# Performance work log

Measured on AMD Instinct MI355X. Metric: run time of the kernel, lower is better.

## Reference

```python
import jax, jax.numpy as jnp
import numpy as np

B, T, D = 2, 2048, 1024
NH, NKV, HD = 16, 4, 64
ROPE = 16  # partial RoPE dims (first 16 of 64)
HALF = ROPE // 2


def apply_rope(x, cos, sin):
    # x: (B, nH, T, HD); rotate first ROPE dims, pass the rest through
    x1 = x[..., :HALF]
    x2 = x[..., HALF:ROPE]
    xp = x[..., ROPE:]
    c = cos[None, None, :, :]  # (1,1,T,HALF)
    s = sin[None, None, :, :]
    return jnp.concatenate([x1 * c - x2 * s, x1 * s + x2 * c, xp], axis=-1)


def setup_inputs() -> dict:
    key = jax.random.key(0)
    k0, k1, k2 = jax.random.split(key, 3)
    x = jax.random.normal(k0, (B, T, D), dtype=jnp.float32)
    # RoPE tables for the rotated sub-dimension (half = ROPE//2 = 8)
    inv_freq = 1.0 / (10000.0 ** (jnp.arange(HALF, dtype=jnp.float32) / HALF))
    ang = jnp.arange(T, dtype=jnp.float32)[:, None] * inv_freq[None, :]
    cos = jnp.cos(ang)
    sin = jnp.sin(ang)
    attn_mask = jnp.tril(jnp.ones((T, T), dtype=bool))  # causal
    w_qkv = jax.random.normal(k1, ((NH + 2 * NKV) * HD, D), dtype=jnp.float32) * (D ** -0.5)
    w_out = jax.random.normal(k2, (D, D), dtype=jnp.float32) * (D ** -0.5)
    q_scale = jnp.full((NH, 1), 1.5, dtype=jnp.float32)
    k_scale = jnp.full((NKV, 1), 1.5, dtype=jnp.float32)
    return {"x": x, "cos": cos, "sin": sin, "attn_mask": attn_mask,
            "w_qkv": w_qkv, "w_out": w_out, "q_scale": q_scale, "k_scale": k_scale}


def reference(x, cos, sin, attn_mask, w_qkv, w_out, q_scale, k_scale):
    Bx, Tx, C = x.shape
    groups = NH // NKV
    qkv = x @ w_qkv.T  # (B,T,(NH+2*NKV)*HD)
    q, k, v = jnp.split(qkv, [NH * HD, (NH + NKV) * HD], axis=-1)
    q = q.reshape(Bx, Tx, NH, HD).transpose(0, 2, 1, 3)    # (B,NH,T,HD)
    k = k.reshape(Bx, Tx, NKV, HD).transpose(0, 2, 1, 3)   # (B,NKV,T,HD)
    v = v.reshape(Bx, Tx, NKV, HD).transpose(0, 2, 1, 3)
    # per-head qk gain scaling
    q = q * q_scale[None, :, :, None]  # (1,NH,1,1)
    k = k * k_scale[None, :, :, None]
    # partial RoPE on q and k
    q = apply_rope(q, cos[:Tx], sin[:Tx])
    k = apply_rope(k, cos[:Tx], sin[:Tx])
    # GQA expand (repeat_interleave along heads)
    ke = jnp.repeat(k, groups, axis=1)  # (B,NH,T,HD)
    ve = jnp.repeat(v, groups, axis=1)
    # scaled dot-product attention with causal mask
    scores = jnp.einsum('bhqd,bhkd->bhqk', q, ke) * (HD ** -0.5)
    scores = jnp.where(attn_mask[None, None], scores, -jnp.inf)
    probs = jax.nn.softmax(scores, axis=-1)
    ao = jnp.einsum('bhqk,bhkd->bhqd', probs, ve)  # (B,NH,T,HD)
    # xsa: subtract self-component along the (shared) kv value direction
    ao_r = ao.reshape(Bx, NKV, groups, Tx, HD)
    vv = v[:, :, None]  # (B,NKV,1,T,HD), broadcasts over groups
    dots = jnp.sum(ao_r * vv, axis=-1, keepdims=True)
    norm = jnp.maximum(jnp.sum(vv * vv, axis=-1, keepdims=True), 1e-8)
    ao = (ao_r - (dots / norm) * vv).reshape(Bx, NH, Tx, HD)
    out = ao.transpose(0, 2, 1, 3).reshape(Bx, Tx, C) @ w_out.T
    return out
```

## Files before the change

kernel.cpp:

```cpp
#include <hip/hip_runtime.h>
#include <hip/hip_bf16.h>

#define NB 2
#define NT 2048
#define ND 1024
#define NHEADS 16
#define NKVH 4
#define HDIM 64
#define QKVD 1536

typedef __attribute__((ext_vector_type(8))) short short8;
typedef __attribute__((ext_vector_type(4))) float floatx4;

#if defined(__has_builtin)
#  if __has_builtin(__builtin_amdgcn_global_load_lds)
#    define HAS_GLL 1
#  endif
#endif
#ifndef HAS_GLL
#  define HAS_GLL 0
#endif

__device__ __forceinline__ void gll16(const void* g, void* l, int lane) {
#if HAS_GLL
  (void)lane;
  __builtin_amdgcn_global_load_lds(
      (const __attribute__((address_space(1))) unsigned int*)g,
      (__attribute__((address_space(3))) unsigned int*)l, 16, 0, 0);
#else
  *(short8*)((short*)l) = *(const short8*)g;
#endif
}

__device__ __forceinline__ unsigned short f2bf(float f) {
  union { float f; unsigned int u; } cv; cv.f = f;
  unsigned int u = cv.u;
  u += 0x7fffu + ((u >> 16) & 1u);
  return (unsigned short)(u >> 16);
}
__device__ __forceinline__ float bf2f(unsigned short u) {
  union { unsigned int u; float f; } cv; cv.u = ((unsigned int)u) << 16; return cv.f;
}

#define N4_X   1048576
#define N4_WQ   393216
#define N4_WO   262144
__global__ __launch_bounds__(256) void cvt_all(
    const float* __restrict__ x, const float* __restrict__ wq,
    const float* __restrict__ wo,
    unsigned short* __restrict__ xb, unsigned short* __restrict__ wqb,
    unsigned short* __restrict__ wob) {
  int i = blockIdx.x * 256 + threadIdx.x;
  const float* src; unsigned short* dst; int j;
  if (i < N4_X)              { src = x;  dst = xb;  j = i; }
  else if (i < N4_X + N4_WQ) { src = wq; dst = wqb; j = i - N4_X; }
  else                       { src = wo; dst = wob; j = i - N4_X - N4_WQ; }
  float4 v = ((const float4*)src)[j];
  ushort4 o;
  o.x = f2bf(v.x); o.y = f2bf(v.y); o.z = f2bf(v.z); o.w = f2bf(v.w);
  ((ushort4*)dst)[j] = o;
}

__global__ __launch_bounds__(256) void gemm_qkv(
    const unsigned short* __restrict__ A,
    const unsigned short* __restrict__ Bm,
    const float* __restrict__ cosT, const float* __restrict__ sinT,
    const float* __restrict__ q_scale, const float* __restrict__ k_scale,
    unsigned short* __restrict__ qb, unsigned short* __restrict__ kb,
    unsigned short* __restrict__ vtb)
{
  const int M = NB * NT, N = QKVD, K = ND;
  __shared__ __align__(16) short As[2][128][32];
  __shared__ __align__(16) short Bs[2][128][32];

  const int tid = threadIdx.x;
  const int wid = tid >> 6, lane = tid & 63;
  const int quad = lane >> 4, l16 = lane & 15;
  const int lo8 = l16 & 7;
  const int wm = (wid >> 1) * 64, wn = (wid & 1) * 64;
  const int m0 = blockIdx.x * 128, n0 = blockIdx.y * 128;

  const int r0 = tid >> 2;
  const int lc = ((tid & 3) ^ (r0 & 3)) * 8;

  const unsigned short* ag0 = A  + (size_t)(m0 + r0) * K + lc;
  const unsigned short* ag1 = ag0 + (size_t)64 * K;
  const unsigned short* bg0 = Bm + (size_t)(n0 + r0) * K + lc;
  const unsigned short* bg1 = bg0 + (size_t)64 * K;

  short* asb = &As[0][0][0];
  short* bsb = &Bs[0][0][0];
  const int lofs = (HAS_GLL ? wid * 512 : tid * 8);
  const int cs = (quad ^ (l16 & 3)) * 8;

  floatx4 acc[4][4] = {};

  gll16(ag0, asb + lofs, lane);
  gll16(ag1, asb + 2048 + lofs, lane);
  gll16(bg0, bsb + lofs, lane);
  gll16(bg1, bsb + 2048 + lofs, lane);

  const int NIT = K / 32;
  for (int it = 0; it < NIT; it++) {
    __syncthreads();
    const int bi = it & 1, bn = bi ^ 1;
    if (it + 1 < NIT) {
      const int k = (it + 1) * 32;
      gll16(ag0 + k, asb + bn * 4096 + lofs, lane);
      gll16(ag1 + k, asb + bn * 4096 + 2048 + lofs, lane);
      gll16(bg0 + k, bsb + bn * 4096 + lofs, lane);
      gll16(bg1 + k, bsb + bn * 4096 + 2048 + lofs, lane);
    }
    short8 af[4], bf[4];
#pragma unroll
    for (int mi = 0; mi < 4; mi++) af[mi] = *(const short8*)&As[bi][wm + mi * 16 + l16][cs];
#pragma unroll
    for (int ni = 0; ni < 4; ni++) bf[ni] = *(const short8*)&Bs[bi][wn + ni * 16 + l16][cs];
#pragma unroll
    for (int mi = 0; mi < 4; mi++)
#pragma unroll
      for (int ni = 0; ni < 4; ni++)
        acc[mi][ni] = __builtin_amdgcn_mfma_f32_16x16x32_bf16(af[mi], bf[ni], acc[mi][ni], 0, 0, 0);
  }

  const int hh = blockIdx.y * 2 + (wid & 1);

  if (hh >= NHEADS + NKVH) {
    const int kvh = hh - (NHEADS + NKVH);
#pragma unroll
    for (int mi = 0; mi < 4; mi++) {
      const int mrow = m0 + wm + mi * 16 + quad * 4;
      const int bb = mrow >> 11, tt = mrow & (NT - 1);
#pragma unroll
      for (int ni = 0; ni < 4; ni++) {
        const int d = ni * 16 + l16;
        ushort4 w;
        w.x = f2bf(acc[mi][ni][0]); w.y = f2bf(acc[mi][ni][1]);
        w.z = f2bf(acc[mi][ni][2]); w.w = f2bf(acc[mi][ni][3]);
        *(ushort4*)(vtb + ((size_t)((bb * NKVH + kvh) * HDIM + d)) * NT + tt) = w;
      }
    }
  } else {
    float scl; unsigned short* dst0; int hloc;
    if (hh < NHEADS) { scl = q_scale[hh] * (0.125f * 1.44269504088896f); hloc = hh; dst0 = qb; }
    else             { scl = k_scale[hh - NHEADS];                        hloc = hh - NHEADS; dst0 = kb; }
    const int nh = (hh < NHEADS) ? NHEADS : NKVH;
#pragma unroll
    for (int mi = 0; mi < 4; mi++) {
#pragma unroll
      for (int r = 0; r < 4; r++) {
        const int mrow = m0 + wm + mi * 16 + quad * 4 + r;
        const int bb = mrow >> 11, tt = mrow & (NT - 1);
        unsigned short* drow = dst0 + ((size_t)((bb * nh + hloc) * NT + tt)) * HDIM;

        const float own = acc[mi][0][r];
        const float oth = __shfl_xor(own, 8);
        const float c = cosT[tt * 8 + lo8], s = sinT[tt * 8 + lo8];
        const float roped = (l16 < 8) ? (own * c - oth * s)
                                      : (oth * s + own * c);
        drow[l16] = f2bf(roped * scl);
#pragma unroll
        for (int ni = 1; ni < 4; ni++)
          drow[ni * 16 + l16] = f2bf(acc[mi][ni][r] * scl);
      }
    }
  }
}

__global__ __launch_bounds__(256) void gemm_lds(
    const unsigned short* __restrict__ A,
    const unsigned short* __restrict__ Bm,
    float* __restrict__ C, int M, int N, int K)
{
  __shared__ __align__(16) short As[2][128][32];
  __shared__ __align__(16) short Bs[2][128][32];

  const int tid = threadIdx.x;
  const int wid = tid >> 6, lane = tid & 63;
  const int quad = lane >> 4, l16 = lane & 15;
  const int wm = (wid >> 1) * 64, wn = (wid & 1) * 64;
  const int m0 = blockIdx.x * 128, n0 = blockIdx.y * 128;

  const int r0 = tid >> 2;
  const int lc = ((tid & 3) ^ (r0 & 3)) * 8;

  const unsigned short* ag0 = A  + (size_t)(m0 + r0) * K + lc;
  const unsigned short* ag1 = ag0 + (size_t)64 * K;
  const unsigned short* bg0 = Bm + (size_t)(n0 + r0) * K + lc;
  const unsigned short* bg1 = bg0 + (size_t)64 * K;

  short* asb = &As[0][0][0];
  short* bsb = &Bs[0][0][0];
  const int lofs = (HAS_GLL ? wid * 512 : tid * 8);
  const int cs = (quad ^ (l16 & 3)) * 8;

  floatx4 acc[4][4] = {};

  gll16(ag0, asb + lofs, lane);
  gll16(ag1, asb + 2048 + lofs, lane);
  gll16(bg0, bsb + lofs, lane);
  gll16(bg1, bsb + 2048 + lofs, lane);

  const int NIT = K / 32;
  for (int it = 0; it < NIT; it++) {
    __syncthreads();
    const int bi = it & 1, bn = bi ^ 1;
    if (it + 1 < NIT) {
      const int k = (it + 1) * 32;
      gll16(ag0 + k, asb + bn * 4096 + lofs, lane);
      gll16(ag1 + k, asb + bn * 4096 + 2048 + lofs, lane);
      gll16(bg0 + k, bsb + bn * 4096 + lofs, lane);
      gll16(bg1 + k, bsb + bn * 4096 + 2048 + lofs, lane);
    }
    short8 af[4], bf[4];
#pragma unroll
    for (int mi = 0; mi < 4; mi++) af[mi] = *(const short8*)&As[bi][wm + mi * 16 + l16][cs];
#pragma unroll
    for (int ni = 0; ni < 4; ni++) bf[ni] = *(const short8*)&Bs[bi][wn + ni * 16 + l16][cs];
#pragma unroll
    for (int mi = 0; mi < 4; mi++)
#pragma unroll
      for (int ni = 0; ni < 4; ni++)
        acc[mi][ni] = __builtin_amdgcn_mfma_f32_16x16x32_bf16(af[mi], bf[ni], acc[mi][ni], 0, 0, 0);
  }

#pragma unroll
  for (int mi = 0; mi < 4; mi++)
#pragma unroll
    for (int ni = 0; ni < 4; ni++)
#pragma unroll
      for (int r = 0; r < 4; r++) {
        int m = m0 + wm + mi * 16 + quad * 4 + r;
        int n = n0 + wn + ni * 16 + l16;
        C[(size_t)m * N + n] = acc[mi][ni][r];
      }
}

__global__ __launch_bounds__(256) void fattn(
    const unsigned short* __restrict__ qb,
    const unsigned short* __restrict__ kb,
    const unsigned short* __restrict__ vtb,
    unsigned short* __restrict__ aob,
    float* __restrict__ pbuf)
{
  const int idx = blockIdx.x;
  const int h = blockIdx.y, b = blockIdx.z;
  const int kv = h >> 2;

  int qt, j0, cnt, chunk; bool direct;
  if (idx < 16) { qt = 16 + idx; j0 = 0; cnt = 16; chunk = 0; direct = false; }
  else {
    int rel = idx - 16, s = 16 - (rel >> 1);
    if ((rel & 1) == 0) { qt = s - 1;  j0 = 0;  cnt = s; chunk = 0; direct = true;  }
    else                { qt = s + 15; j0 = 16; cnt = s; chunk = 1; direct = false; }
  }

  const int tid = threadIdx.x;
  const int wid = tid >> 6, lane = tid & 63;
  const int quad = lane >> 4, l16 = lane & 15;
  const int hi8 = l16 >> 3, lo8 = l16 & 7;

  __shared__ __align__(16) short Ks[2][64][64];
  __shared__ __align__(16) short Vs[2][64][64];
  __shared__ __align__(16) short Ps[4][16][64];

  const unsigned short* qg = qb + ((size_t)((b * NHEADS + h) * NT + qt * 64)) * HDIM;
  const int qrow = wid * 16 + l16;
  short8 aq0 = *(const short8*)(qg + (size_t)qrow * HDIM + quad * 8);
  short8 aq1 = *(const short8*)(qg + (size_t)qrow * HDIM + 32 + quad * 8);

  const int sr  = tid >> 3;
  const int lck = ((tid & 7) ^ (sr & 7)) * 8;
  const unsigned short* kgp0 = kb  + ((size_t)((b * NKVH + kv) * NT) + sr) * HDIM + lck;
  const unsigned short* vgp0 = vtb + ((size_t)((b * NKVH + kv) * HDIM) + sr) * NT + lck;
  short* ksb = &Ks[0][0][0];
  short* vsb = &Vs[0][0][0];
  const int lofs = (HAS_GLL ? wid * 512 : tid * 8);

  const int cs0 = (quad ^ lo8) * 8;
  const int cs1 = cs0 ^ 32;

  int pwo[4][4];
#pragma unroll
  for (int r = 0; r < 4; r++) {
    const int row = quad * 4 + r;
#pragma unroll
    for (int nb = 0; nb < 4; nb++)
      pwo[r][nb] = wid * 1024 + row * 64 + (((nb * 2 + hi8) ^ (row & 7)) * 8) + lo8;
  }
  short* psf = &Ps[0][0][0];

  floatx4 acc_o[4] = {};
  float lsum[4] = {0.f, 0.f, 0.f, 0.f};

  {
    const unsigned short* kg = kgp0 + (size_t)j0 * 64 * HDIM;
    const unsigned short* vg = vgp0 + j0 * 64;
    gll16(kg, ksb + lofs, lane);
    gll16(kg + 32 * HDIM, ksb + 2048 + lofs, lane);
    gll16(vg, vsb + lofs, lane);
    gll16(vg + (size_t)32 * NT, vsb + 2048 + lofs, lane);
  }

  for (int i = 0; i < cnt; i++) {
    const int jt = j0 + i;
    __syncthreads();
    const int bi = i & 1, bn = bi ^ 1;
    if (i + 1 < cnt) {
      const unsigned short* kg = kgp0 + (size_t)(jt + 1) * 64 * HDIM;
      const unsigned short* vg = vgp0 + (jt + 1) * 64;
      gll16(kg, ksb + bn * 4096 + lofs, lane);
      gll16(kg + 32 * HDIM, ksb + bn * 4096 + 2048 + lofs, lane);
      gll16(vg, vsb + bn * 4096 + lofs, lane);
      gll16(vg + (size_t)32 * NT, vsb + bn * 4096 + 2048 + lofs, lane);
    }

    floatx4 s[4] = {};
#pragma unroll
    for (int nb = 0; nb < 4; nb++) {
      short8 bk0 = *(const short8*)&Ks[bi][nb * 16 + l16][cs0];
      short8 bk1 = *(const short8*)&Ks[bi][nb * 16 + l16][cs1];
      s[nb] = __builtin_amdgcn_mfma_f32_16x16x32_bf16(aq0, bk0, s[nb], 0, 0, 0);
      s[nb] = __builtin_amdgcn_mfma_f32_16x16x32_bf16(aq1, bk1, s[nb], 0, 0, 0);
    }

    if (jt == qt) {
#pragma unroll
      for (int nb = 0; nb < 4; nb++) {
        int col = nb * 16 + l16;
#pragma unroll
        for (int r = 0; r < 4; r++)
          if (col > wid * 16 + quad * 4 + r) s[nb][r] = -INFINITY;
      }
    }

#pragma unroll
    for (int r = 0; r < 4; r++) {
#pragma unroll
      for (int nb = 0; nb < 4; nb++) {
        float p = __builtin_amdgcn_exp2f(s[nb][r]);
        lsum[r] += p;
        psf[pwo[r][nb]] = (short)(__float_as_uint(p) >> 16);
      }
    }

    short8 ap0 = *(const short8*)&Ps[wid][l16][cs0];
    short8 ap1 = *(const short8*)&Ps[wid][l16][cs1];
#pragma unroll
    for (int nb = 0; nb < 4; nb++) {
      short8 bv0 = *(const short8*)&Vs[bi][nb * 16 + l16][cs0];
      short8 bv1 = *(const short8*)&Vs[bi][nb * 16 + l16][cs1];
      acc_o[nb] = __builtin_amdgcn_mfma_f32_16x16x32_bf16(ap0, bv0, acc_o[nb], 0, 0, 0);
      acc_o[nb] = __builtin_amdgcn_mfma_f32_16x16x32_bf16(ap1, bv1, acc_o[nb], 0, 0, 0);
    }
  }

  const int bl = (cnt - 1) & 1;

  if (direct) {
#pragma unroll
    for (int r = 0; r < 4; r++) {
      float ls = lsum[r];
#pragma unroll
      for (int off = 1; off < 16; off <<= 1) ls += __shfl_xor(ls, off);
      const float invl = 1.f / ls;

      const int rowl = wid * 16 + quad * 4 + r;
      const int vcol = ((rowl >> 3) ^ lo8) * 8 + (rowl & 7);
      float vd[4], dot = 0.f, vv = 0.f;
#pragma unroll
      for (int nb = 0; nb < 4; nb++) {
        vd[nb] = bf2f((unsigned short)Vs[bl][nb * 16 + l16][vcol]);
        dot += acc_o[nb][r] * invl * vd[nb];
        vv  += vd[nb] * vd[nb];
      }
#pragma unroll
      for (int off = 1; off < 16; off <<= 1) {
        dot += __shfl_xor(dot, off);
        vv  += __shfl_xor(vv, off);
      }
      const float coef = dot / fmaxf(vv, 1e-8f);
      unsigned short* dst = aob + ((size_t)(b * NT + qt * 64 + rowl)) * ND + h * HDIM + l16;
#pragma unroll
      for (int nb = 0; nb < 4; nb++)
        dst[nb * 16] = f2bf(acc_o[nb][r] * invl - coef * vd[nb]);
    }
  } else {
    const int slot = ((b * NHEADS + h) * 16 + (qt - 16)) * 2 + chunk;
    float* pO = pbuf + (size_t)slot * 4160;
    float* pl = pO + 4096;
#pragma unroll
    for (int r = 0; r < 4; r++) {
      float ls = lsum[r];
#pragma unroll
      for (int off = 1; off < 16; off <<= 1) ls += __shfl_xor(ls, off);
      const int rowl = wid * 16 + quad * 4 + r;
      if (l16 == 0) pl[rowl] = ls;
#pragma unroll
      for (int nb = 0; nb < 4; nb++)
        pO[rowl * 64 + nb * 16 + l16] = acc_o[nb][r];
    }
  }
}

__global__ __launch_bounds__(256) void redn(
    const float* __restrict__ pbuf,
    const unsigned short* __restrict__ vtb,
    unsigned short* __restrict__ aob)
{
  const int qt = 16 + blockIdx.x;
  const int h = blockIdx.y, b = blockIdx.z;
  const int kv = h >> 2;
  const int tid = threadIdx.x;

  const int slot0 = ((b * NHEADS + h) * 16 + blockIdx.x) * 2;
  const float* O0 = pbuf + (size_t)slot0 * 4160;
  const float* O1 = O0 + 4160;
  const float* l0 = O0 + 4096;
  const float* l1 = O1 + 4096;

  __shared__ short vt[64][66];

  {
    const int d = tid >> 2, tq = (tid & 3) * 16;
    const unsigned short* src = vtb + ((size_t)((b * NKVH + kv) * HDIM + d)) * NT + qt * 64 + tq;
    short8 v0 = *(const short8*)src;
    short8 v1 = *(const short8*)(src + 8);
    *(short8*)&vt[d][tq] = v0;
    *(short8*)&vt[d][tq + 8] = v1;
  }
  __syncthreads();

  const int row = tid >> 2, dq = tid & 3;
  const float invl = 1.f / (l0[row] + l1[row]);

  float o[16], vd[16];
  float dot = 0.f, vv = 0.f;
#pragma unroll
  for (int j = 0; j < 16; j++) {
    const int d = dq * 16 + j;
    float ov = (O0[row * 64 + d] + O1[row * 64 + d]) * invl;
    float v  = bf2f((unsigned short)vt[d][row]);
    o[j] = ov; vd[j] = v;
    dot += ov * v; vv += v * v;
  }
  dot += __shfl_xor(dot, 1); dot += __shfl_xor(dot, 2);
  vv  += __shfl_xor(vv, 1);  vv  += __shfl_xor(vv, 2);
  const float coef = dot / fmaxf(vv, 1e-8f);

  unsigned short* dst = aob + ((size_t)(b * NT + qt * 64 + row)) * ND + h * HDIM + dq * 16;
  ushort4 w0, w1, w2, w3;
  w0.x = f2bf(o[0] - coef * vd[0]);  w0.y = f2bf(o[1] - coef * vd[1]);
  w0.z = f2bf(o[2] - coef * vd[2]);  w0.w = f2bf(o[3] - coef * vd[3]);
  w1.x = f2bf(o[4] - coef * vd[4]);  w1.y = f2bf(o[5] - coef * vd[5]);
  w1.z = f2bf(o[6] - coef * vd[6]);  w1.w = f2bf(o[7] - coef * vd[7]);
  w2.x = f2bf(o[8] - coef * vd[8]);  w2.y = f2bf(o[9] - coef * vd[9]);
  w2.z = f2bf(o[10] - coef * vd[10]); w2.w = f2bf(o[11] - coef * vd[11]);
  w3.x = f2bf(o[12] - coef * vd[12]); w3.y = f2bf(o[13] - coef * vd[13]);
  w3.z = f2bf(o[14] - coef * vd[14]); w3.w = f2bf(o[15] - coef * vd[15]);
  ((ushort4*)dst)[0] = w0; ((ushort4*)dst)[1] = w1;
  ((ushort4*)dst)[2] = w2; ((ushort4*)dst)[3] = w3;
}

extern "C" void kernel_launch(void* const* d_in, const int* in_sizes, int n_in,
                              void* d_out, int out_size, void* d_ws, size_t ws_size,
                              hipStream_t stream) {
  const float* x       = (const float*)d_in[0];
  const float* cosT    = (const float*)d_in[1];
  const float* sinT    = (const float*)d_in[2];
  const float* w_qkv   = (const float*)d_in[4];
  const float* w_out   = (const float*)d_in[5];
  const float* q_scale = (const float*)d_in[6];
  const float* k_scale = (const float*)d_in[7];
  float* out = (float*)d_out;

  char* ws = (char*)d_ws;
  unsigned short* xb    = (unsigned short*)ws;
  unsigned short* wqkvb = (unsigned short*)(ws + 8388608);
  float*          pbuf  = (float*)ws;
  unsigned short* woutb = (unsigned short*)(ws + 17825792);
  unsigned short* qb    = (unsigned short*)(ws + 19922944);
  unsigned short* kb    = (unsigned short*)(ws + 28311552);
  unsigned short* vtb   = (unsigned short*)(ws + 30408704);
  unsigned short* aob   = (unsigned short*)(ws + 32505856);

  cvt_all<<<(N4_X + N4_WQ + N4_WO) / 256, 256, 0, stream>>>(
      x, w_qkv, w_out, xb, wqkvb, woutb);

  gemm_qkv<<<dim3(NB * NT / 128, QKVD / 128), 256, 0, stream>>>(
      xb, wqkvb, cosT, sinT, q_scale, k_scale, qb, kb, vtb);

  fattn<<<dim3(48, NHEADS, NB), 256, 0, stream>>>(qb, kb, vtb, aob, pbuf);
  redn<<<dim3(16, NHEADS, NB), 256, 0, stream>>>(pbuf, vtb, aob);

  gemm_lds<<<dim3(NB * NT / 128, ND / 128), 256, 0, stream>>>(
      aob, woutb, out, NB * NT, ND, ND);
}
```

Measured before the change: 195.2 us.

## Shrink GEMM N-tiles to 64 and pair query heads per attention block

Both GEMMs now use 128x64 tiles in which each wave owns 32 rows across the full 64 columns, which doubles the grid and gives the 256-CU part more blocks. The QKV GEMM now maps one head per block column. The attention kernel now has each block handle two query heads that share a KV head, with each wave doing 32 query rows, so every K/V tile staged in LDS is used by twice as many MFMAs. The trade-off is fewer attention blocks, twice the Ps LDS footprint, and more registers per wave, which may lower occupancy.

```diff
diff --git a/kernel.cpp b/kernel.cpp
--- a/kernel.cpp
+++ b/kernel.cpp
@@ -69,16 +69,16 @@
     unsigned short* __restrict__ qb, unsigned short* __restrict__ kb,
     unsigned short* __restrict__ vtb)
 {
-  const int M = NB * NT, N = QKVD, K = ND;
+  const int K = ND;
   __shared__ __align__(16) short As[2][128][32];
-  __shared__ __align__(16) short Bs[2][128][32];
+  __shared__ __align__(16) short Bs[2][64][32];
 
   const int tid = threadIdx.x;
   const int wid = tid >> 6, lane = tid & 63;
   const int quad = lane >> 4, l16 = lane & 15;
   const int lo8 = l16 & 7;
-  const int wm = (wid >> 1) * 64, wn = (wid & 1) * 64;
-  const int m0 = blockIdx.x * 128, n0 = blockIdx.y * 128;
+  const int wm = wid * 32;
+  const int m0 = blockIdx.x * 128, n0 = blockIdx.y * 64;
 
   const int r0 = tid >> 2;
   const int lc = ((tid & 3) ^ (r0 & 3)) * 8;
@@ -86,19 +86,17 @@
   const unsigned short* ag0 = A  + (size_t)(m0 + r0) * K + lc;
   const unsigned short* ag1 = ag0 + (size_t)64 * K;
   const unsigned short* bg0 = Bm + (size_t)(n0 + r0) * K + lc;
-  const unsigned short* bg1 = bg0 + (size_t)64 * K;
 
   short* asb = &As[0][0][0];
   short* bsb = &Bs[0][0][0];
   const int lofs = (HAS_GLL ? wid * 512 : tid * 8);
   const int cs = (quad ^ (l16 & 3)) * 8;
 
-  floatx4 acc[4][4] = {};
+  floatx4 acc[2][4] = {};
 
   gll16(ag0, asb + lofs, lane);
   gll16(ag1, asb + 2048 + lofs, lane);
   gll16(bg0, bsb + lofs, lane);
-  gll16(bg1, bsb + 2048 + lofs, lane);
 
   const int NIT = K / 32;
   for (int it = 0; it < NIT; it++) {
@@ -108,27 +106,26 @@
       const int k = (it + 1) * 32;
       gll16(ag0 + k, asb + bn * 4096 + lofs, lane);
       gll16(ag1 + k, asb + bn * 4096 + 2048 + lofs, lane);
-      gll16(bg0 + k, bsb + bn * 4096 + lofs, lane);
-      gll16(bg1 + k, bsb + bn * 4096 + 2048 + lofs, lane);
-    }
-    short8 af[4], bf[4];
-#pragma unroll
-    for (int mi = 0; mi < 4; mi++) af[mi] = *(const short8*)&As[bi][wm + mi * 16 + l16][cs];
-#pragma unroll
-    for (int ni = 0; ni < 4; ni++) bf[ni] = *(const short8*)&Bs[bi][wn + ni * 16 + l16][cs];
-#pragma unroll
-    for (int mi = 0; mi < 4; mi++)
+      gll16(bg0 + k, bsb + bn * 2048 + lofs, lane);
+    }
+    short8 af[2], bf[4];
+#pragma unroll
+    for (int mi = 0; mi < 2; mi++) af[mi] = *(const short8*)&As[bi][wm + mi * 16 + l16][cs];
+#pragma unroll
+    for (int ni = 0; ni < 4; ni++) bf[ni] = *(const short8*)&Bs[bi][ni * 16 + l16][cs];
+#pragma unroll
+    for (int mi = 0; mi < 2; mi++)
 #pragma unroll
       for (int ni = 0; ni < 4; ni++)
         acc[mi][ni] = __builtin_amdgcn_mfma_f32_16x16x32_bf16(af[mi], bf[ni], acc[mi][ni], 0, 0, 0);
   }
 
-  const int hh = blockIdx.y * 2 + (wid & 1);
+  const int hh = blockIdx.y;
 
   if (hh >= NHEADS + NKVH) {
     const int kvh = hh - (NHEADS + NKVH);
 #pragma unroll
-    for (int mi = 0; mi < 4; mi++) {
+    for (int mi = 0; mi < 2; mi++) {
       const int mrow = m0 + wm + mi * 16 + quad * 4;
       const int bb = mrow >> 11, tt = mrow & (NT - 1);
 #pragma unroll
@@ -141,12 +138,11 @@
       }
     }
   } else {
-    float scl; unsigned short* dst0; int hloc;
-    if (hh < NHEADS) { scl = q_scale[hh] * (0.125f * 1.44269504088896f); hloc = hh; dst0 = qb; }
-    else             { scl = k_scale[hh - NHEADS];                        hloc = hh - NHEADS; dst0 = kb; }
-    const int nh = (hh < NHEADS) ? NHEADS : NKVH;
-#pragma unroll
-    for (int mi = 0; mi < 4; mi++) {
+    float scl; unsigned short* dst0; int hloc, nh;
+    if (hh < NHEADS) { scl = q_scale[hh] * (0.125f * 1.44269504088896f); hloc = hh; dst0 = qb; nh = NHEADS; }
+    else             { scl = k_scale[hh - NHEADS]; hloc = hh - NHEADS; dst0 = kb; nh = NKVH; }
+#pragma unroll
+    for (int mi = 0; mi < 2; mi++) {
 #pragma unroll
       for (int r = 0; r < 4; r++) {
         const int mrow = m0 + wm + mi * 16 + quad * 4 + r;
@@ -167,19 +163,19 @@
   }
 }
 
-__global__ __launch_bounds__(256) void gemm_lds(
+__global__ __launch_bounds__(256) void gemm_out(
     const unsigned short* __restrict__ A,
     const unsigned short* __restrict__ Bm,
     float* __restrict__ C, int M, int N, int K)
 {
   __shared__ __align__(16) short As[2][128][32];
-  __shared__ __align__(16) short Bs[2][128][32];
+  __shared__ __align__(16) short Bs[2][64][32];
 
   const int tid = threadIdx.x;
   const int wid = tid >> 6, lane = tid & 63;
   const int quad = lane >> 4, l16 = lane & 15;
-  const int wm = (wid >> 1) * 64, wn = (wid & 1) * 64;
-  const int m0 = blockIdx.x * 128, n0 = blockIdx.y * 128;
+  const int wm = wid * 32;
+  const int m0 = blockIdx.x * 128, n0 = blockIdx.y * 64;
 
   const int r0 = tid >> 2;
   const int lc = ((tid & 3) ^ (r0 & 3)) * 8;
@@ -187,19 +183,17 @@
   const unsigned short* ag0 = A  + (size_t)(m0 + r0) * K + lc;
   const unsigned short* ag1 = ag0 + (size_t)64 * K;
   const unsigned short* bg0 = Bm + (size_t)(n0 + r0) * K + lc;
-  const unsigned short* bg1 = bg0 + (size_t)64 * K;
 
   short* asb = &As[0][0][0];
   short* bsb = &Bs[0][0][0];
   const int lofs = (HAS_GLL ? wid * 512 : tid * 8);
   const int cs = (quad ^ (l16 & 3)) * 8;
 
-  floatx4 acc[4][4] = {};
+  floatx4 acc[2][4] = {};
 
   gll16(ag0, asb + lofs, lane);
   gll16(ag1, asb + 2048 + lofs, lane);
   gll16(bg0, bsb + lofs, lane);
-  gll16(bg1, bsb + 2048 + lofs, lane);
 
   const int NIT = K / 32;
   for (int it = 0; it < NIT; it++) {
@@ -209,29 +203,28 @@
       const int k = (it + 1) * 32;
       gll16(ag0 + k, asb + bn * 4096 + lofs, lane);
       gll16(ag1 + k, asb + bn * 4096 + 2048 + lofs, lane);
-      gll16(bg0 + k, bsb + bn * 4096 + lofs, lane);
-      gll16(bg1 + k, bsb + bn * 4096 + 2048 + lofs, lane);
-    }
-    short8 af[4], bf[4];
-#pragma unroll
-    for (int mi = 0; mi < 4; mi++) af[mi] = *(const short8*)&As[bi][wm + mi * 16 + l16][cs];
-#pragma unroll
-    for (int ni = 0; ni < 4; ni++) bf[ni] = *(const short8*)&Bs[bi][wn + ni * 16 + l16][cs];
-#pragma unroll
-    for (int mi = 0; mi < 4; mi++)
+      gll16(bg0 + k, bsb + bn * 2048 + lofs, lane);
+    }
+    short8 af[2], bf[4];
+#pragma unroll
+    for (int mi = 0; mi < 2; mi++) af[mi] = *(const short8*)&As[bi][wm + mi * 16 + l16][cs];
+#pragma unroll
+    for (int ni = 0; ni < 4; ni++) bf[ni] = *(const short8*)&Bs[bi][ni * 16 + l16][cs];
+#pragma unroll
+    for (int mi = 0; mi < 2; mi++)
 #pragma unroll
       for (int ni = 0; ni < 4; ni++)
         acc[mi][ni] = __builtin_amdgcn_mfma_f32_16x16x32_bf16(af[mi], bf[ni], acc[mi][ni], 0, 0, 0);
   }
 
 #pragma unroll
-  for (int mi = 0; mi < 4; mi++)
+  for (int mi = 0; mi < 2; mi++)
 #pragma unroll
     for (int ni = 0; ni < 4; ni++)
 #pragma unroll
       for (int r = 0; r < 4; r++) {
         int m = m0 + wm + mi * 16 + quad * 4 + r;
-        int n = n0 + wn + ni * 16 + l16;
+        int n = n0 + ni * 16 + l16;
         C[(size_t)m * N + n] = acc[mi][ni][r];
       }
 }
@@ -244,8 +237,8 @@
     float* __restrict__ pbuf)
 {
   const int idx = blockIdx.x;
-  const int h = blockIdx.y, b = blockIdx.z;
-  const int kv = h >> 2;
+  const int p = blockIdx.y, b = blockIdx.z;
+  const int h0 = p * 2, kv = p >> 1;
 
   int qt, j0, cnt, chunk; bool direct;
   if (idx < 16) { qt = 16 + idx; j0 = 0; cnt = 16; chunk = 0; direct = false; }
@@ -259,15 +252,21 @@
   const int wid = tid >> 6, lane = tid & 63;
   const int quad = lane >> 4, l16 = lane & 15;
   const int hi8 = l16 >> 3, lo8 = l16 & 7;
+  const int hw = h0 + (wid >> 1);
+  const int half = wid & 1;
 
   __shared__ __align__(16) short Ks[2][64][64];
   __shared__ __align__(16) short Vs[2][64][64];
-  __shared__ __align__(16) short Ps[4][16][64];
-
-  const unsigned short* qg = qb + ((size_t)((b * NHEADS + h) * NT + qt * 64)) * HDIM;
-  const int qrow = wid * 16 + l16;
-  short8 aq0 = *(const short8*)(qg + (size_t)qrow * HDIM + quad * 8);
-  short8 aq1 = *(const short8*)(qg + (size_t)qrow * HDIM + 32 + quad * 8);
+  __shared__ __align__(16) short Ps[4][32][64];
+
+  short8 aq[2][2];
+#pragma unroll
+  for (int s = 0; s < 2; s++) {
+    const unsigned short* qg = qb +
+        ((size_t)((b * NHEADS + hw) * NT + qt * 64 + half * 32 + s * 16 + l16)) * HDIM;
+    aq[s][0] = *(const short8*)(qg + quad * 8);
+    aq[s][1] = *(const short8*)(qg + 32 + quad * 8);
+  }
 
   const int sr  = tid >> 3;
   const int lck = ((tid & 7) ^ (sr & 7)) * 8;
@@ -286,12 +285,12 @@
     const int row = quad * 4 + r;
 #pragma unroll
     for (int nb = 0; nb < 4; nb++)
-      pwo[r][nb] = wid * 1024 + row * 64 + (((nb * 2 + hi8) ^ (row & 7)) * 8) + lo8;
+      pwo[r][nb] = wid * 2048 + row * 64 + (((nb * 2 + hi8) ^ (row & 7)) * 8) + lo8;
   }
   short* psf = &Ps[0][0][0];
 
-  floatx4 acc_o[4] = {};
-  float lsum[4] = {0.f, 0.f, 0.f, 0.f};
+  floatx4 acc_o[2][4] = {};
+  float lsum[2][4] = {};
 
   {
     const unsigned short* kg = kgp0 + (size_t)j0 * 64 * HDIM;
@@ -315,43 +314,56 @@
       gll16(vg + (size_t)32 * NT, vsb + bn * 4096 + 2048 + lofs, lane);
     }
 
-    floatx4 s[4] = {};
+    floatx4 sa[2][4] = {};
 #pragma unroll
     for (int nb = 0; nb < 4; nb++) {
       short8 bk0 = *(const short8*)&Ks[bi][nb * 16 + l16][cs0];
       short8 bk1 = *(const short8*)&Ks[bi][nb * 16 + l16][cs1];
-      s[nb] = __builtin_amdgcn_mfma_f32_16x16x32_bf16(aq0, bk0, s[nb], 0, 0, 0);
-      s[nb] = __builtin_amdgcn_mfma_f32_16x16x32_bf16(aq1, bk1, s[nb], 0, 0, 0);
+#pragma unroll
+      for (int s = 0; s < 2; s++) {
+        sa[s][nb] = __builtin_amdgcn_mfma_f32_16x16x32_bf16(aq[s][0], bk0, sa[s][nb], 0, 0, 0);
+        sa[s][nb] = __builtin_amdgcn_mfma_f32_16x16x32_bf16(aq[s][1], bk1, sa[s][nb], 0, 0, 0);
+      }
     }
 
     if (jt == qt) {
 #pragma unroll
-      for (int nb = 0; nb < 4; nb++) {
-        int col = nb * 16 + l16;
-#pragma unroll
-        for (int r = 0; r < 4; r++)
-          if (col > wid * 16 + quad * 4 + r) s[nb][r] = -INFINITY;
-      }
-    }
-
-#pragma unroll
-    for (int r = 0; r < 4; r++) {
-#pragma unroll
-      for (int nb = 0; nb < 4; nb++) {
-        float p = __builtin_amdgcn_exp2f(s[nb][r]);
-        lsum[r] += p;
-        psf[pwo[r][nb]] = (short)(__float_as_uint(p) >> 16);
-      }
-    }
-
-    short8 ap0 = *(const short8*)&Ps[wid][l16][cs0];
-    short8 ap1 = *(const short8*)&Ps[wid][l16][cs1];
+      for (int s = 0; s < 2; s++)
+#pragma unroll
+        for (int nb = 0; nb < 4; nb++) {
+          int col = nb * 16 + l16;
+#pragma unroll
+          for (int r = 0; r < 4; r++)
+            if (col > half * 32 + s * 16 + quad * 4 + r) sa[s][nb][r] = -INFINITY;
+        }
+    }
+
+#pragma unroll
+    for (int s = 0; s < 2; s++)
+#pragma unroll
+      for (int r = 0; r < 4; r++)
+#pragma unroll
+        for (int nb = 0; nb < 4; nb++) {
+          float pv = __builtin_amdgcn_exp2f(sa[s][nb][r]);
+          lsum[s][r] += pv;
+          psf[s * 1024 + pwo[r][nb]] = (short)(__float_as_uint(pv) >> 16);
+        }
+
+    short8 ap[2][2];
+#pragma unroll
+    for (int s = 0; s < 2; s++) {
+      ap[s][0] = *(const short8*)(psf + wid * 2048 + s * 1024 + l16 * 64 + cs0);
+      ap[s][1] = *(const short8*)(psf + wid * 2048 + s * 1024 + l16 * 64 + cs1);
+    }
 #pragma unroll
     for (int nb = 0; nb < 4; nb++) {
       short8 bv0 = *(const short8*)&Vs[bi][nb * 16 + l16][cs0];
       short8 bv1 = *(const short8*)&Vs[bi][nb * 16 + l16][cs1];
-      acc_o[nb] = __builtin_amdgcn_mfma_f32_16x16x32_bf16(ap0, bv0, acc_o[nb], 0, 0, 0);
-      acc_o[nb] = __builtin_amdgcn_mfma_f32_16x16x32_bf16(ap1, bv1, acc_o[nb], 0, 0, 0);
+#pragma unroll
+      for (int s = 0; s < 2; s++) {
+        acc_o[s][nb] = __builtin_amdgcn_mfma_f32_16x16x32_bf16(ap[s][0], bv0, acc_o[s][nb], 0, 0, 0);
+        acc_o[s][nb] = __builtin_amdgcn_mfma_f32_16x16x32_bf16(ap[s][1], bv1, acc_o[s][nb], 0, 0, 0);
+      }
     }
   }
 
@@ -359,47 +371,51 @@
 
   if (direct) {
 #pragma unroll
-    for (int r = 0; r < 4; r++) {
-      float ls = lsum[r];
-#pragma unroll
-      for (int off = 1; off < 16; off <<= 1) ls += __shfl_xor(ls, off);
-      const float invl = 1.f / ls;
-
-      const int rowl = wid * 16 + quad * 4 + r;
-      const int vcol = ((rowl >> 3) ^ lo8) * 8 + (rowl & 7);
-      float vd[4], dot = 0.f, vv = 0.f;
-#pragma unroll
-      for (int nb = 0; nb < 4; nb++) {
-        vd[nb] = bf2f((unsigned short)Vs[bl][nb * 16 + l16][vcol]);
-        dot += acc_o[nb][r] * invl * vd[nb];
-        vv  += vd[nb] * vd[nb];
-      }
-#pragma unroll
-      for (int off = 1; off < 16; off <<= 1) {
-        dot += __shfl_xor(dot, off);
-        vv  += __shfl_xor(vv, off);
-      }
-      const float coef = dot / fmaxf(vv, 1e-8f);
-      unsigned short* dst = aob + ((size_t)(b * NT + qt * 64 + rowl)) * ND + h * HDIM + l16;
-#pragma unroll
-      for (int nb = 0; nb < 4; nb++)
-        dst[nb * 16] = f2bf(acc_o[nb][r] * invl - coef * vd[nb]);
-    }
+    for (int s = 0; s < 2; s++)
+#pragma unroll
+      for (int r = 0; r < 4; r++) {
+        float ls = lsum[s][r];
+#pragma unroll
+        for (int off = 1; off < 16; off <<= 1) ls += __shfl_xor(ls, off);
+        const float invl = 1.f / ls;
+
+        const int rowl = half * 32 + s * 16 + quad * 4 + r;
+        const int vcol = ((rowl >> 3) ^ lo8) * 8 + (rowl & 7);
+        float vd[4], dot = 0.f, vv = 0.f;
+#pragma unroll
+        for (int nb = 0; nb < 4; nb++) {
+          vd[nb] = bf2f((unsigned short)Vs[bl][nb * 16 + l16][vcol]);
+          dot += acc_o[s][nb][r] * invl * vd[nb];
+          vv  += vd[nb] * vd[nb];
+        }
+#pragma unroll
+        for (int off = 1; off < 16; off <<= 1) {
+          dot += __shfl_xor(dot, off);
+          vv  += __shfl_xor(vv, off);
+        }
+        const float coef = dot / fmaxf(vv, 1e-8f);
+        unsigned short* dst = aob + ((size_t)(b * NT + qt * 64 + rowl)) * ND + hw * HDIM + l16;
+#pragma unroll
+        for (int nb = 0; nb < 4; nb++)
+          dst[nb * 16] = f2bf(acc_o[s][nb][r] * invl - coef * vd[nb]);
+      }
   } else {
-    const int slot = ((b * NHEADS + h) * 16 + (qt - 16)) * 2 + chunk;
+    const int slot = ((b * NHEADS + hw) * 16 + (qt - 16)) * 2 + chunk;
     float* pO = pbuf + (size_t)slot * 4160;
     float* pl = pO + 4096;
 #pragma unroll
-    for (int r = 0; r < 4; r++) {
-      float ls = lsum[r];
-#pragma unroll
-      for (int off = 1; off < 16; off <<= 1) ls += __shfl_xor(ls, off);
-      const int rowl = wid * 16 + quad * 4 + r;
-      if (l16 == 0) pl[rowl] = ls;
-#pragma unroll
-      for (int nb = 0; nb < 4; nb++)
-        pO[rowl * 64 + nb * 16 + l16] = acc_o[nb][r];
-    }
+    for (int s = 0; s < 2; s++)
+#pragma unroll
+      for (int r = 0; r < 4; r++) {
+        float ls = lsum[s][r];
+#pragma unroll
+        for (int off = 1; off < 16; off <<= 1) ls += __shfl_xor(ls, off);
+        const int rowl = half * 32 + s * 16 + quad * 4 + r;
+        if (l16 == 0) pl[rowl] = ls;
+#pragma unroll
+        for (int nb = 0; nb < 4; nb++)
+          pO[rowl * 64 + nb * 16 + l16] = acc_o[s][nb][r];
+      }
   }
 }
 
@@ -487,12 +503,12 @@
   cvt_all<<<(N4_X + N4_WQ + N4_WO) / 256, 256, 0, stream>>>(
       x, w_qkv, w_out, xb, wqkvb, woutb);
 
-  gemm_qkv<<<dim3(NB * NT / 128, QKVD / 128), 256, 0, stream>>>(
+  gemm_qkv<<<dim3(NB * NT / 128, QKVD / 64), 256, 0, stream>>>(
       xb, wqkvb, cosT, sinT, q_scale, k_scale, qb, kb, vtb);
 
-  fattn<<<dim3(48, NHEADS, NB), 256, 0, stream>>>(qb, kb, vtb, aob, pbuf);
+  fattn<<<dim3(48, NHEADS / 2, NB), 256, 0, stream>>>(qb, kb, vtb, aob, pbuf);
   redn<<<dim3(16, NHEADS, NB), 256, 0, stream>>>(pbuf, vtb, aob);
 
-  gemm_lds<<<dim3(NB * NT / 128, ND / 128), 256, 0, stream>>>(
+  gemm_out<<<dim3(NB * NT / 128, ND / 64), 256, 0, stream>>>(
       aob, woutb, out, NB * NT, ND, ND);
 }
```

Result: no change. 195.2 us (+0.0%).

## Split GEMM blocks into single-wave 64x64 tiles for more blocks

Applied to the files above, without the earlier changes.

Both projection GEMMs now run one wave per block on a 64x64 output tile instead of four waves sharing a 128x128 tile, with the shared main loop factored into a macro. Block count grows fourfold, which spreads work over more CUs (the 128-tile grid gave only 384 and 256 blocks on a 256-CU part) and removes the intra-block barrier cost across waves. In exchange each A/B tile is loaded from global/L2 by more blocks, since reuse per loaded byte drops by half.

```diff
diff --git a/kernel.cpp b/kernel.cpp
--- a/kernel.cpp
+++ b/kernel.cpp
@@ -61,7 +61,51 @@
   ((ushort4*)dst)[j] = o;
 }
 
-__global__ __launch_bounds__(256) void gemm_qkv(
+
+#define GEMM1W_PROLOGUE(Aptr, Bptr, Kdim)                                      \
+  __shared__ __align__(16) short As[2][64][32];                                \
+  __shared__ __align__(16) short Bs[2][64][32];                                \
+  const int lane = threadIdx.x;                                                \
+  const int quad = lane >> 4, l16 = lane & 15;                                 \
+  const int srow = lane >> 2;                                                  \
+  const int sch  = ((lane & 3) ^ (srow & 3)) * 8;                              \
+  const unsigned short* agp = (Aptr) + (size_t)(m0 + srow) * (Kdim) + sch;     \
+  const unsigned short* bgp = (Bptr) + (size_t)(n0 + srow) * (Kdim) + sch;     \
+  short* asb = &As[0][0][0];                                                   \
+  short* bsb = &Bs[0][0][0];                                                   \
+  const int lofs = (HAS_GLL ? 0 : lane * 8);                                   \
+  const int cs = (quad ^ (l16 & 3)) * 8;                                       \
+  floatx4 acc[4][4] = {};                                                      \
+  _Pragma("unroll")                                                            \
+  for (int g = 0; g < 4; g++) {                                                \
+    gll16(agp + (size_t)(16 * g) * (Kdim), asb + g * 512 + lofs, lane);        \
+    gll16(bgp + (size_t)(16 * g) * (Kdim), bsb + g * 512 + lofs, lane);        \
+  }                                                                            \
+  const int NIT = (Kdim) / 32;                                                 \
+  for (int it = 0; it < NIT; it++) {                                           \
+    __syncthreads();                                                           \
+    const int bi = it & 1, bn = bi ^ 1;                                        \
+    if (it + 1 < NIT) {                                                        \
+      const int k = (it + 1) * 32;                                             \
+      _Pragma("unroll")                                                        \
+      for (int g = 0; g < 4; g++) {                                            \
+        gll16(agp + (size_t)(16 * g) * (Kdim) + k, asb + bn * 2048 + g * 512 + lofs, lane); \
+        gll16(bgp + (size_t)(16 * g) * (Kdim) + k, bsb + bn * 2048 + g * 512 + lofs, lane); \
+      }                                                                        \
+    }                                                                          \
+    short8 af[4], bf[4];                                                       \
+    _Pragma("unroll")                                                          \
+    for (int mi = 0; mi < 4; mi++) af[mi] = *(const short8*)&As[bi][mi * 16 + l16][cs]; \
+    _Pragma("unroll")                                                          \
+    for (int ni = 0; ni < 4; ni++) bf[ni] = *(const short8*)&Bs[bi][ni * 16 + l16][cs]; \
+    _Pragma("unroll")                                                          \
+    for (int mi = 0; mi < 4; mi++)                                             \
+      _Pragma("unroll")                                                        \
+      for (int ni = 0; ni < 4; ni++)                                           \
+        acc[mi][ni] = __builtin_amdgcn_mfma_f32_16x16x32_bf16(af[mi], bf[ni], acc[mi][ni], 0, 0, 0); \
+  }
+
+__global__ __launch_bounds__(64) void gemm_qkv(
     const unsigned short* __restrict__ A,
     const unsigned short* __restrict__ Bm,
     const float* __restrict__ cosT, const float* __restrict__ sinT,
@@ -69,67 +113,17 @@
     unsigned short* __restrict__ qb, unsigned short* __restrict__ kb,
     unsigned short* __restrict__ vtb)
 {
-  const int M = NB * NT, N = QKVD, K = ND;
-  __shared__ __align__(16) short As[2][128][32];
-  __shared__ __align__(16) short Bs[2][128][32];
-
-  const int tid = threadIdx.x;
-  const int wid = tid >> 6, lane = tid & 63;
-  const int quad = lane >> 4, l16 = lane & 15;
+  const int m0 = blockIdx.x * 64, n0 = blockIdx.y * 64;
+  GEMM1W_PROLOGUE(A, Bm, ND)
+
+  const int hh = blockIdx.y;
   const int lo8 = l16 & 7;
-  const int wm = (wid >> 1) * 64, wn = (wid & 1) * 64;
-  const int m0 = blockIdx.x * 128, n0 = blockIdx.y * 128;
-
-  const int r0 = tid >> 2;
-  const int lc = ((tid & 3) ^ (r0 & 3)) * 8;
-
-  const unsigned short* ag0 = A  + (size_t)(m0 + r0) * K + lc;
-  const unsigned short* ag1 = ag0 + (size_t)64 * K;
-  const unsigned short* bg0 = Bm + (size_t)(n0 + r0) * K + lc;
-  const unsigned short* bg1 = bg0 + (size_t)64 * K;
-
-  short* asb = &As[0][0][0];
-  short* bsb = &Bs[0][0][0];
-  const int lofs = (HAS_GLL ? wid * 512 : tid * 8);
-  const int cs = (quad ^ (l16 & 3)) * 8;
-
-  floatx4 acc[4][4] = {};
-
-  gll16(ag0, asb + lofs, lane);
-  gll16(ag1, asb + 2048 + lofs, lane);
-  gll16(bg0, bsb + lofs, lane);
-  gll16(bg1, bsb + 2048 + lofs, lane);
-
-  const int NIT = K / 32;
-  for (int it = 0; it < NIT; it++) {
-    __syncthreads();
-    const int bi = it & 1, bn = bi ^ 1;
-    if (it + 1 < NIT) {
-      const int k = (it + 1) * 32;
-      gll16(ag0 + k, asb + bn * 4096 + lofs, lane);
-      gll16(ag1 + k, asb + bn * 4096 + 2048 + lofs, lane);
-      gll16(bg0 + k, bsb + bn * 4096 + lofs, lane);
-      gll16(bg1 + k, bsb + bn * 4096 + 2048 + lofs, lane);
-    }
-    short8 af[4], bf[4];
-#pragma unroll
-    for (int mi = 0; mi < 4; mi++) af[mi] = *(const short8*)&As[bi][wm + mi * 16 + l16][cs];
-#pragma unroll
-    for (int ni = 0; ni < 4; ni++) bf[ni] = *(const short8*)&Bs[bi][wn + ni * 16 + l16][cs];
-#pragma unroll
-    for (int mi = 0; mi < 4; mi++)
-#pragma unroll
-      for (int ni = 0; ni < 4; ni++)
-        acc[mi][ni] = __builtin_amdgcn_mfma_f32_16x16x32_bf16(af[mi], bf[ni], acc[mi][ni], 0, 0, 0);
-  }
-
-  const int hh = blockIdx.y * 2 + (wid & 1);
 
   if (hh >= NHEADS + NKVH) {
     const int kvh = hh - (NHEADS + NKVH);
 #pragma unroll
     for (int mi = 0; mi < 4; mi++) {
-      const int mrow = m0 + wm + mi * 16 + quad * 4;
+      const int mrow = m0 + mi * 16 + quad * 4;
       const int bb = mrow >> 11, tt = mrow & (NT - 1);
 #pragma unroll
       for (int ni = 0; ni < 4; ni++) {
@@ -141,15 +135,14 @@
       }
     }
   } else {
-    float scl; unsigned short* dst0; int hloc;
-    if (hh < NHEADS) { scl = q_scale[hh] * (0.125f * 1.44269504088896f); hloc = hh; dst0 = qb; }
-    else             { scl = k_scale[hh - NHEADS];                        hloc = hh - NHEADS; dst0 = kb; }
-    const int nh = (hh < NHEADS) ? NHEADS : NKVH;
+    float scl; unsigned short* dst0; int hloc, nh;
+    if (hh < NHEADS) { scl = q_scale[hh] * (0.125f * 1.44269504088896f); hloc = hh; dst0 = qb; nh = NHEADS; }
+    else             { scl = k_scale[hh - NHEADS]; hloc = hh - NHEADS; dst0 = kb; nh = NKVH; }
 #pragma unroll
     for (int mi = 0; mi < 4; mi++) {
 #pragma unroll
       for (int r = 0; r < 4; r++) {
-        const int mrow = m0 + wm + mi * 16 + quad * 4 + r;
+        const int mrow = m0 + mi * 16 + quad * 4 + r;
         const int bb = mrow >> 11, tt = mrow & (NT - 1);
         unsigned short* drow = dst0 + ((size_t)((bb * nh + hloc) * NT + tt)) * HDIM;
 
@@ -167,62 +160,13 @@
   }
 }
 
-__global__ __launch_bounds__(256) void gemm_lds(
+__global__ __launch_bounds__(64) void gemm_out(
     const unsigned short* __restrict__ A,
     const unsigned short* __restrict__ Bm,
     float* __restrict__ C, int M, int N, int K)
 {
-  __shared__ __align__(16) short As[2][128][32];
-  __shared__ __align__(16) short Bs[2][128][32];
-
-  const int tid = threadIdx.x;
-  const int wid = tid >> 6, lane = tid & 63;
-  const int quad = lane >> 4, l16 = lane & 15;
-  const int wm = (wid >> 1) * 64, wn = (wid & 1) * 64;
-  const int m0 = blockIdx.x * 128, n0 = blockIdx.y * 128;
-
-  const int r0 = tid >> 2;
-  const int lc = ((tid & 3) ^ (r0 & 3)) * 8;
-
-  const unsigned short* ag0 = A  + (size_t)(m0 + r0) * K + lc;
-  const unsigned short* ag1 = ag0 + (size_t)64 * K;
-  const unsigned short* bg0 = Bm + (size_t)(n0 + r0) * K + lc;
-  const unsigned short* bg1 = bg0 + (size_t)64 * K;
-
-  short* asb = &As[0][0][0];
-  short* bsb = &Bs[0][0][0];
-  const int lofs = (HAS_GLL ? wid * 512 : tid * 8);
-  const int cs = (quad ^ (l16 & 3)) * 8;
-
-  floatx4 acc[4][4] = {};
-
-  gll16(ag0, asb + lofs, lane);
-  gll16(ag1, asb + 2048 + lofs, lane);
-  gll16(bg0, bsb + lofs, lane);
-  gll16(bg1, bsb + 2048 + lofs, lane);
-
-  const int NIT = K / 32;
-  for (int it = 0; it < NIT; it++) {
-    __syncthreads();
-    const int bi = it & 1, bn = bi ^ 1;
-    if (it + 1 < NIT) {
-      const int k = (it + 1) * 32;
-      gll16(ag0 + k, asb + bn * 4096 + lofs, lane);
-      gll16(ag1 + k, asb + bn * 4096 + 2048 + lofs, lane);
-      gll16(bg0 + k, bsb + bn * 4096 + lofs, lane);
-      gll16(bg1 + k, bsb + bn * 4096 + 2048 + lofs, lane);
-    }
-    short8 af[4], bf[4];
-#pragma unroll
-    for (int mi = 0; mi < 4; mi++) af[mi] = *(const short8*)&As[bi][wm + mi * 16 + l16][cs];
-#pragma unroll
-    for (int ni = 0; ni < 4; ni++) bf[ni] = *(const short8*)&Bs[bi][wn + ni * 16 + l16][cs];
-#pragma unroll
-    for (int mi = 0; mi < 4; mi++)
-#pragma unroll
-      for (int ni = 0; ni < 4; ni++)
-        acc[mi][ni] = __builtin_amdgcn_mfma_f32_16x16x32_bf16(af[mi], bf[ni], acc[mi][ni], 0, 0, 0);
-  }
+  const int m0 = blockIdx.x * 64, n0 = blockIdx.y * 64;
+  GEMM1W_PROLOGUE(A, Bm, K)
 
 #pragma unroll
   for (int mi = 0; mi < 4; mi++)
@@ -230,8 +174,8 @@
     for (int ni = 0; ni < 4; ni++)
 #pragma unroll
       for (int r = 0; r < 4; r++) {
-        int m = m0 + wm + mi * 16 + quad * 4 + r;
-        int n = n0 + wn + ni * 16 + l16;
+        int m = m0 + mi * 16 + quad * 4 + r;
+        int n = n0 + ni * 16 + l16;
         C[(size_t)m * N + n] = acc[mi][ni][r];
       }
 }
@@ -487,12 +431,12 @@
   cvt_all<<<(N4_X + N4_WQ + N4_WO) / 256, 256, 0, stream>>>(
       x, w_qkv, w_out, xb, wqkvb, woutb);
 
-  gemm_qkv<<<dim3(NB * NT / 128, QKVD / 128), 256, 0, stream>>>(
+  gemm_qkv<<<dim3(NB * NT / 64, QKVD / 64), 64, 0, stream>>>(
       xb, wqkvb, cosT, sinT, q_scale, k_scale, qb, kb, vtb);
 
   fattn<<<dim3(48, NHEADS, NB), 256, 0, stream>>>(qb, kb, vtb, aob, pbuf);
   redn<<<dim3(16, NHEADS, NB), 256, 0, stream>>>(pbuf, vtb, aob);
 
-  gemm_lds<<<dim3(NB * NT / 128, ND / 128), 256, 0, stream>>>(
+  gemm_out<<<dim3(NB * NT / 64, ND / 64), 64, 0, stream>>>(
       aob, woutb, out, NB * NT, ND, ND);
 }
```

After: 193.5 us. About the same (-0.9%).
